# Optimization experiments

Measured on AMD Instinct MI355X. Metric: run time of the kernel, lower is better.

Reference implementation:

```python
import jax, jax.numpy as jnp
from jax import lax
import numpy as np

SIGMA = 1.0
TRUNCATE = 3.0

def _gaussian_1d(sigma, truncate):
    tail = int(sigma * truncate)
    x = np.arange(-tail, tail + 1, dtype=np.float32)
    k = np.exp(-0.5 * x * x / (sigma * sigma))
    k = k / k.sum()
    return jnp.asarray(k, dtype=jnp.float32)  # length 2*tail+1 (=7)


def setup_inputs() -> dict:
    key = jax.random.key(0)
    image = jax.random.normal(key, (2, 160, 160, 160, 4), dtype=jnp.float32)
    return {"image": image}


def reference(image):
    # Separable per-channel (depthwise) Gaussian blur along each spatial axis,
    # SAME padding, stride 1 -- identical math to the TF per-channel conv loop.
    k = _gaussian_1d(SIGMA, TRUNCATE)
    K = k.shape[0]
    C = image.shape[-1]
    out = image
    for d in range(3):  # spatial axes D, H, W
        kshape = [1, 1, 1]
        kshape[d] = K
        # depthwise kernel: (kd, kh, kw, in_per_group=1, C)
        rhs = jnp.broadcast_to(k.reshape(kshape + [1, 1]), tuple(kshape) + (1, C))
        out = lax.conv_general_dilated(
            out, rhs,
            window_strides=(1, 1, 1),
            padding='SAME',
            dimension_numbers=('NDHWC', 'DHWIO', 'NDHWC'),
            feature_group_count=C,
        )
    return out
```

## Files before the change

### kernel.cpp

```cpp
#include <hip/hip_runtime.h>


#define THT 16
#define TWT 16
#define CHUNK 16
#define NS (CHUNK + 6)
#define DIM 160
#define SLICE (DIM * DIM)
#define HALON (22 * 22)
#define NBLK 2000

#define W0 0.004433048f
#define W1 0.054005582f
#define W2 0.242036229f
#define W3 0.399050300f

__device__ __forceinline__ float4 blur7(float4 a0, float4 a1, float4 a2, float4 a3,
                                        float4 a4, float4 a5, float4 a6) {
    float4 r;
    r.x = W0 * (a0.x + a6.x) + W1 * (a1.x + a5.x) + W2 * (a2.x + a4.x) + W3 * a3.x;
    r.y = W0 * (a0.y + a6.y) + W1 * (a1.y + a5.y) + W2 * (a2.y + a4.y) + W3 * a3.y;
    r.z = W0 * (a0.z + a6.z) + W1 * (a1.z + a5.z) + W2 * (a2.z + a4.z) + W3 * a3.z;
    r.w = W0 * (a0.w + a6.w) + W1 * (a1.w + a5.w) + W2 * (a2.w + a4.w) + W3 * a3.w;
    return r;
}

__global__ __launch_bounds__(64, 2)
void gauss3d_fused(const float4* __restrict__ in, float4* __restrict__ out) {
    const int bid = blockIdx.x;
    int wid = (bid & 7) * (NBLK / 8) + (bid >> 3);

    const int lane = threadIdx.x;

    const int tw    = wid % 10;  wid /= 10;
    const int th    = wid % 10;  wid /= 10;
    const int chunk = wid % 10;  wid /= 10;
    const int n     = wid;

    const int h0 = th * THT;
    const int w0 = tw * TWT;
    const int d0 = chunk * CHUNK;

    __shared__ float4 raw[22][23];
    __shared__ float4 wb[22][17];

    const size_t nbase = (size_t)n * DIM * SLICE;
    const float4 z = make_float4(0.f, 0.f, 0.f, 0.f);

    int  soff[8], ridx[8];
    bool sok[8];
    #pragma unroll
    for (int s = 0; s < 8; ++s) {
        const int j = lane + 64 * s;
        const bool has = (j < HALON);
        const int rr = has ? (j / 22) : 0, cc = has ? (j % 22) : 0;
        const int gh = h0 + rr - 3, gw = w0 + cc - 3;
        const bool ok = has && gh >= 0 && gh < DIM && gw >= 0 && gw < DIM;
        soff[s] = ok ? (gh * DIM + gw) : 0;
        sok[s]  = ok;
        ridx[s] = rr * 23 + cc;
    }
    const bool has7 = (lane + 448 < HALON);

    const int g1r = lane >> 2, g1c = (lane & 3) * 4;
    const bool hasG2 = (lane < 24);
    const int g2r = (64 + lane) >> 2, g2c = ((64 + lane) & 3) * 4;

    const int q  = lane >> 4;
    const int lw = lane & 15;

    float4 qa0=z,qa1=z,qa2=z,qa3=z,qa4=z,qa5=z,qa6=z;
    float4 qb0=z,qb1=z,qb2=z,qb3=z,qb4=z,qb5=z,qb6=z;
    float4 qc0=z,qc1=z,qc2=z,qc3=z,qc4=z,qc5=z,qc6=z;
    float4 qd0=z,qd1=z,qd2=z,qd3=z,qd4=z,qd5=z,qd6=z;

    float4 pf0, pf1, pf2, pf3, pf4, pf5, pf6, pf7;

#define PREFETCH(DSL)                                                        \
    do {                                                                     \
        const int _d = (DSL);                                                \
        const bool _inr = (_d >= 0) && (_d < DIM);                           \
        const float4* _s = in + nbase + (size_t)(_inr ? _d : 0) * SLICE;     \
        pf0 = (_inr && sok[0]) ? _s[soff[0]] : z;                            \
        pf1 = (_inr && sok[1]) ? _s[soff[1]] : z;                            \
        pf2 = (_inr && sok[2]) ? _s[soff[2]] : z;                            \
        pf3 = (_inr && sok[3]) ? _s[soff[3]] : z;                            \
        pf4 = (_inr && sok[4]) ? _s[soff[4]] : z;                            \
        pf5 = (_inr && sok[5]) ? _s[soff[5]] : z;                            \
        pf6 = (_inr && sok[6]) ? _s[soff[6]] : z;                            \
        pf7 = (_inr && sok[7]) ? _s[soff[7]] : z;                            \
    } while (0)

#define WGRP(R, C0)                                                          \
    do {                                                                     \
        const float4* _rr = &raw[R][0];                                      \
        float4 v0 = _rr[(C0) + 0];                                           \
        float4 v1 = _rr[(C0) + 1];                                           \
        float4 v2 = _rr[(C0) + 2];                                           \
        float4 v3 = _rr[(C0) + 3];                                           \
        float4 v4 = _rr[(C0) + 4];                                           \
        float4 v5 = _rr[(C0) + 5];                                           \
        float4 v6 = _rr[(C0) + 6];                                           \
        float4 v7 = _rr[(C0) + 7];                                           \
        float4 v8 = _rr[(C0) + 8];                                           \
        float4 v9 = _rr[(C0) + 9];                                           \
        float4* _wr = &wb[R][0];                                             \
        _wr[(C0) + 0] = blur7(v0, v1, v2, v3, v4, v5, v6);                   \
        _wr[(C0) + 1] = blur7(v1, v2, v3, v4, v5, v6, v7);                   \
        _wr[(C0) + 2] = blur7(v2, v3, v4, v5, v6, v7, v8);                   \
        _wr[(C0) + 3] = blur7(v3, v4, v5, v6, v7, v8, v9);                   \
    } while (0)

    PREFETCH(d0 - 3);

    for (int k = 0; k < NS; ++k) {
        const int din = d0 - 3 + k;

        {
            float4* rb = &raw[0][0];
            rb[ridx[0]] = pf0;
            rb[ridx[1]] = pf1;
            rb[ridx[2]] = pf2;
            rb[ridx[3]] = pf3;
            rb[ridx[4]] = pf4;
            rb[ridx[5]] = pf5;
            rb[ridx[6]] = pf6;
            if (has7) rb[ridx[7]] = pf7;
        }

        if (k + 1 < NS) PREFETCH(din + 1);

        WGRP(g1r, g1c);
        if (hasG2) WGRP(g2r, g2c);

        {
            float4 t0 = wb[4 * q + 0][lw];
            float4 t1 = wb[4 * q + 1][lw];
            float4 t2 = wb[4 * q + 2][lw];
            float4 t3 = wb[4 * q + 3][lw];
            float4 t4 = wb[4 * q + 4][lw];
            float4 t5 = wb[4 * q + 5][lw];
            float4 t6 = wb[4 * q + 6][lw];
            float4 t7 = wb[4 * q + 7][lw];
            float4 t8 = wb[4 * q + 8][lw];
            float4 t9 = wb[4 * q + 9][lw];
            float4 va = blur7(t0, t1, t2, t3, t4, t5, t6);
            float4 vb = blur7(t1, t2, t3, t4, t5, t6, t7);
            float4 vc = blur7(t2, t3, t4, t5, t6, t7, t8);
            float4 vd = blur7(t3, t4, t5, t6, t7, t8, t9);
            qa0=qa1; qa1=qa2; qa2=qa3; qa3=qa4; qa4=qa5; qa5=qa6; qa6=va;
            qb0=qb1; qb1=qb2; qb2=qb3; qb3=qb4; qb4=qb5; qb5=qb6; qb6=vb;
            qc0=qc1; qc1=qc2; qc2=qc3; qc3=qc4; qc4=qc5; qc5=qc6; qc6=vc;
            qd0=qd1; qd1=qd2; qd2=qd3; qd3=qd4; qd4=qd5; qd5=qd6; qd6=vd;
        }

        if (k >= 6) {
            const int dout = din - 3;
            float4 oa = blur7(qa0, qa1, qa2, qa3, qa4, qa5, qa6);
            float4 ob = blur7(qb0, qb1, qb2, qb3, qb4, qb5, qb6);
            float4 oc = blur7(qc0, qc1, qc2, qc3, qc4, qc5, qc6);
            float4 od = blur7(qd0, qd1, qd2, qd3, qd4, qd5, qd6);
            const size_t base = nbase + (size_t)dout * SLICE + (size_t)(h0 + 4 * q) * DIM + (w0 + lw);
            out[base + 0 * DIM] = oa;
            out[base + 1 * DIM] = ob;
            out[base + 2 * DIM] = oc;
            out[base + 3 * DIM] = od;
        }
    }
#undef PREFETCH
#undef WGRP
}

extern "C" void kernel_launch(void* const* d_in, const int* in_sizes, int n_in,
                              void* d_out, int out_size, void* d_ws, size_t ws_size,
                              hipStream_t stream) {
    const float4* in = (const float4*)d_in[0];
    float4* out = (float4*)d_out;
    gauss3d_fused<<<NBLK, 64, 0, stream>>>(in, out);
}
```

Baseline: 72.84 us.

## Stage halo slices directly into double-buffered LDS via global_load_lds

Replaces the register prefetch followed by an LDS store with `__builtin_amdgcn_global_load_lds` 16-byte loads that write each depth slice straight into shared memory. The halo buffer is double-buffered so the next slice lands while the current one is blurred. Explicit `s_waitcnt vmcnt` waits replace the implicit register dependency. Out-of-range halo cells are zero-filled once in LDS, and out-of-range depth slices are zero-filled per stage. The aim is to cut VGPR pressure and the extra LDS write pass. The cost is relying on hand-counted vmcnt ordering, which assumes the four output stores per iteration are the only later memory operations.

```diff
diff --git a/kernel.cpp b/kernel.cpp
--- a/kernel.cpp
+++ b/kernel.cpp
@@ -7,7 +7,8 @@
 #define NS (CHUNK + 6)
 #define DIM 160
 #define SLICE (DIM * DIM)
-#define HALON (22 * 22)
+#define RSTR 23
+#define RTOT (22 * RSTR)
 #define NBLK 2000
 
 #define W0 0.004433048f
@@ -23,6 +24,13 @@
     r.z = W0 * (a0.z + a6.z) + W1 * (a1.z + a5.z) + W2 * (a2.z + a4.z) + W3 * a3.z;
     r.w = W0 * (a0.w + a6.w) + W1 * (a1.w + a5.w) + W2 * (a2.w + a4.w) + W3 * a3.w;
     return r;
+}
+
+typedef __attribute__((address_space(3))) void lds_void_t;
+typedef const __attribute__((address_space(1))) void gbl_void_t;
+
+__device__ __forceinline__ void gload16(const float4* g, float4* l) {
+    __builtin_amdgcn_global_load_lds((gbl_void_t*)g, (lds_void_t*)l, 16, 0, 0);
 }
 
 __global__ __launch_bounds__(64, 2)
@@ -41,30 +49,39 @@
     const int w0 = tw * TWT;
     const int d0 = chunk * CHUNK;
 
-    __shared__ float4 raw[22][23];
+    __shared__ float4 raw[2][512];
     __shared__ float4 wb[22][17];
 
     const size_t nbase = (size_t)n * DIM * SLICE;
     const float4 z = make_float4(0.f, 0.f, 0.f, 0.f);
 
-    int  soff[8], ridx[8];
-    bool sok[8];
+    int  soff[8];
+    bool sok[8], rreal[8];
     #pragma unroll
     for (int s = 0; s < 8; ++s) {
         const int j = lane + 64 * s;
-        const bool has = (j < HALON);
-        const int rr = has ? (j / 22) : 0, cc = has ? (j % 22) : 0;
+        const int rr = j / RSTR, cc = j % RSTR;
+        const bool real = (j < RTOT) && (cc < 22);
         const int gh = h0 + rr - 3, gw = w0 + cc - 3;
-        const bool ok = has && gh >= 0 && gh < DIM && gw >= 0 && gw < DIM;
-        soff[s] = ok ? (gh * DIM + gw) : 0;
-        sok[s]  = ok;
-        ridx[s] = rr * 23 + cc;
+        const bool ok = real && gh >= 0 && gh < DIM && gw >= 0 && gw < DIM;
+        soff[s]  = ok ? (gh * DIM + gw) : 0;
+        sok[s]   = ok;
+        rreal[s] = real;
     }
-    const bool has7 = (lane + 448 < HALON);
+
+    #pragma unroll
+    for (int s = 0; s < 8; ++s) {
+        if (rreal[s] && !sok[s]) {
+            raw[0][lane + 64 * s] = z;
+            raw[1][lane + 64 * s] = z;
+        }
+    }
 
     const int g1r = lane >> 2, g1c = (lane & 3) * 4;
     const bool hasG2 = (lane < 24);
     const int g2r = (64 + lane) >> 2, g2c = ((64 + lane) & 3) * 4;
+    const int w1base = g1r * RSTR + g1c;
+    const int w2base = g2r * RSTR + g2c;
 
     const int q  = lane >> 4;
     const int lw = lane & 15;
@@ -74,36 +91,45 @@
     float4 qc0=z,qc1=z,qc2=z,qc3=z,qc4=z,qc5=z,qc6=z;
     float4 qd0=z,qd1=z,qd2=z,qd3=z,qd4=z,qd5=z,qd6=z;
 
-    float4 pf0, pf1, pf2, pf3, pf4, pf5, pf6, pf7;
-
-#define PREFETCH(DSL)                                                        \
+#define STAGE(BUF, DSL)                                                      \
     do {                                                                     \
         const int _d = (DSL);                                                \
-        const bool _inr = (_d >= 0) && (_d < DIM);                           \
-        const float4* _s = in + nbase + (size_t)(_inr ? _d : 0) * SLICE;     \
-        pf0 = (_inr && sok[0]) ? _s[soff[0]] : z;                            \
-        pf1 = (_inr && sok[1]) ? _s[soff[1]] : z;                            \
-        pf2 = (_inr && sok[2]) ? _s[soff[2]] : z;                            \
-        pf3 = (_inr && sok[3]) ? _s[soff[3]] : z;                            \
-        pf4 = (_inr && sok[4]) ? _s[soff[4]] : z;                            \
-        pf5 = (_inr && sok[5]) ? _s[soff[5]] : z;                            \
-        pf6 = (_inr && sok[6]) ? _s[soff[6]] : z;                            \
-        pf7 = (_inr && sok[7]) ? _s[soff[7]] : z;                            \
+        if (_d >= 0 && _d < DIM) {                                           \
+            const float4* _g = in + nbase + (size_t)_d * SLICE;              \
+            float4* _l = &raw[BUF][0];                                       \
+            if (sok[0]) gload16(_g + soff[0], _l + 0);                       \
+            if (sok[1]) gload16(_g + soff[1], _l + 64);                      \
+            if (sok[2]) gload16(_g + soff[2], _l + 128);                     \
+            if (sok[3]) gload16(_g + soff[3], _l + 192);                     \
+            if (sok[4]) gload16(_g + soff[4], _l + 256);                     \
+            if (sok[5]) gload16(_g + soff[5], _l + 320);                     \
+            if (sok[6]) gload16(_g + soff[6], _l + 384);                     \
+            if (sok[7]) gload16(_g + soff[7], _l + 448);                     \
+        } else {                                                             \
+            if (rreal[0]) raw[BUF][lane + 0]   = z;                          \
+            if (rreal[1]) raw[BUF][lane + 64]  = z;                          \
+            if (rreal[2]) raw[BUF][lane + 128] = z;                          \
+            if (rreal[3]) raw[BUF][lane + 192] = z;                          \
+            if (rreal[4]) raw[BUF][lane + 256] = z;                          \
+            if (rreal[5]) raw[BUF][lane + 320] = z;                          \
+            if (rreal[6]) raw[BUF][lane + 384] = z;                          \
+            if (rreal[7]) raw[BUF][lane + 448] = z;                          \
+        }                                                                    \
     } while (0)
 
-#define WGRP(R, C0)                                                          \
+#define WGRP(BASE, R, C0)                                                    \
     do {                                                                     \
-        const float4* _rr = &raw[R][0];                                      \
-        float4 v0 = _rr[(C0) + 0];                                           \
-        float4 v1 = _rr[(C0) + 1];                                           \
-        float4 v2 = _rr[(C0) + 2];                                           \
-        float4 v3 = _rr[(C0) + 3];                                           \
-        float4 v4 = _rr[(C0) + 4];                                           \
-        float4 v5 = _rr[(C0) + 5];                                           \
-        float4 v6 = _rr[(C0) + 6];                                           \
-        float4 v7 = _rr[(C0) + 7];                                           \
-        float4 v8 = _rr[(C0) + 8];                                           \
-        float4 v9 = _rr[(C0) + 9];                                           \
+        const float4* _rr = &raw[buf][BASE];                                 \
+        float4 v0 = _rr[0];                                                  \
+        float4 v1 = _rr[1];                                                  \
+        float4 v2 = _rr[2];                                                  \
+        float4 v3 = _rr[3];                                                  \
+        float4 v4 = _rr[4];                                                  \
+        float4 v5 = _rr[5];                                                  \
+        float4 v6 = _rr[6];                                                  \
+        float4 v7 = _rr[7];                                                  \
+        float4 v8 = _rr[8];                                                  \
+        float4 v9 = _rr[9];                                                  \
         float4* _wr = &wb[R][0];                                             \
         _wr[(C0) + 0] = blur7(v0, v1, v2, v3, v4, v5, v6);                   \
         _wr[(C0) + 1] = blur7(v1, v2, v3, v4, v5, v6, v7);                   \
@@ -111,27 +137,19 @@
         _wr[(C0) + 3] = blur7(v3, v4, v5, v6, v7, v8, v9);                   \
     } while (0)
 
-    PREFETCH(d0 - 3);
+    STAGE(0, d0 - 3);
 
+    int buf = 0;
     for (int k = 0; k < NS; ++k) {
         const int din = d0 - 3 + k;
 
-        {
-            float4* rb = &raw[0][0];
-            rb[ridx[0]] = pf0;
-            rb[ridx[1]] = pf1;
-            rb[ridx[2]] = pf2;
-            rb[ridx[3]] = pf3;
-            rb[ridx[4]] = pf4;
-            rb[ridx[5]] = pf5;
-            rb[ridx[6]] = pf6;
-            if (has7) rb[ridx[7]] = pf7;
-        }
+        if (k <= 6) { asm volatile("s_waitcnt vmcnt(0)" ::: "memory"); }
+        else        { asm volatile("s_waitcnt vmcnt(4)" ::: "memory"); }
 
-        if (k + 1 < NS) PREFETCH(din + 1);
+        if (k + 1 < NS) STAGE(buf ^ 1, din + 1);
 
-        WGRP(g1r, g1c);
-        if (hasG2) WGRP(g2r, g2c);
+        WGRP(w1base, g1r, g1c);
+        if (hasG2) WGRP(w2base, g2r, g2c);
 
         {
             float4 t0 = wb[4 * q + 0][lw];
@@ -166,8 +184,9 @@
             out[base + 2 * DIM] = oc;
             out[base + 3 * DIM] = od;
         }
+        buf ^= 1;
     }
-#undef PREFETCH
+#undef STAGE
 #undef WGRP
 }
 
```

Result: slower. 106.1 us (+45.6%).
